# Kernel tuning notes

Measured on AMD Instinct MI355X. Metric: run time of the kernel, lower is better.

## Reference

```python
import jax, jax.numpy as jnp
import numpy as np

T = 2048            # flattened tokens (vLLM style)
D = 4096            # hidden_size
NSSM = 128          # ssm_state_size
K = 4               # conv kernel size
G = 8               # n_groups
H = 128             # mamba_num_heads
P = 64              # mamba_head_dim
INTER = H * P       # 8192 = expand * hidden_size
CONV_DIM = INTER + 2 * G * NSSM   # 10240 (x, B, C share the conv)
PROJ = INTER + CONV_DIM + H       # 18560 (z, xBC, dt)
Q = 128             # SSD chunk size
EPS = 1e-5


def setup_inputs() -> dict:
    key = jax.random.key(0)
    ks = jax.random.split(key, 9)
    s = 0.02
    return {
        "hidden_states": jax.random.normal(ks[0], (T, D), jnp.float32),
        "residual": jax.random.normal(ks[1], (T, D), jnp.float32),
        "norm_w": jnp.ones((D,), jnp.float32),
        "in_proj_w": jax.random.normal(ks[2], (PROJ, D), jnp.float32) * s,
        "conv_w": jax.random.normal(ks[3], (CONV_DIM, K), jnp.float32) * 0.2,
        "conv_b": jax.random.normal(ks[4], (CONV_DIM,), jnp.float32) * 0.1,
        "A_log": jnp.log(jax.random.uniform(ks[5], (H,), jnp.float32, 1.0, 16.0)),
        "D_res": jax.random.normal(ks[6], (H,), jnp.float32) * 0.5 + 1.0,
        "dt_bias": jax.random.normal(ks[7], (H,), jnp.float32) * 0.5,
        "gn_w": jnp.ones((INTER,), jnp.float32),
        "out_proj_w": jax.random.normal(ks[8], (D, INTER), jnp.float32) * s,
    }


def _forward(hidden_states, residual, norm_w, in_proj_w, conv_w, conv_b,
             A_log, D_res, dt_bias, gn_w, out_proj_w):
    # ---- fused add + RMSNorm (vLLM RMSNorm(hidden, residual)) ----
    resid = hidden_states + residual
    hs = resid * jax.lax.rsqrt(jnp.mean(resid * resid, -1, keepdims=True) + EPS) * norm_w

    # ---- MambaMixer2 ----
    proj = hs @ in_proj_w.T                              # [T, PROJ]
    z, xBC, dt = jnp.split(proj, [INTER, INTER + CONV_DIM], axis=-1)

    # causal depthwise conv1d over time + SiLU
    xp = jnp.pad(xBC, ((K - 1, 0), (0, 0)))
    conv = conv_b + sum(conv_w[:, k] * xp[k:k + T] for k in range(K))
    xBC = jax.nn.silu(conv)

    x, B, C = jnp.split(xBC, [INTER, INTER + G * NSSM], axis=-1)
    x = x.reshape(T, H, P)
    Bh = jnp.repeat(B.reshape(T, G, NSSM), H // G, axis=1)   # [T,H,N]
    Ch = jnp.repeat(C.reshape(T, G, NSSM), H // G, axis=1)   # [T,H,N]

    dt = jax.nn.softplus(dt + dt_bias)                   # [T,H]
    A = -jnp.exp(A_log)                                  # [H] (negative)

    # ---- SSD chunked selective scan ----
    NC = T // Q
    a = (dt * A).reshape(NC, Q, H)                       # per-step log decay (<=0)
    cum = jnp.cumsum(a, axis=1)                          # inclusive cumsum, [NC,Q,H]
    Xd = (dt[:, :, None] * x).reshape(NC, Q, H, P)
    Bc = Bh.reshape(NC, Q, H, NSSM)
    Cc = Ch.reshape(NC, Q, H, NSSM)

    # intra-chunk: Y[i] = sum_{j<=i} (C_i.B_j) exp(cum_i-cum_j) Xd_j
    CB = jnp.einsum('cqhn,ckhn->chqk', Cc, Bc)
    cumT = cum.transpose(0, 2, 1)                        # [NC,H,Q]
    mask = jnp.tril(jnp.ones((Q, Q), bool))
    Lm = jnp.where(mask, jnp.exp(cumT[:, :, :, None] - cumT[:, :, None, :]), 0.0)
    Y = jnp.einsum('chqk,ckhp->cqhp', CB * Lm, Xd)

    # chunk-local end states, then scan states across chunks
    cum_end = cum[:, -1]                                 # [NC,H]
    decay_out = jnp.exp(cum_end[:, None] - cum)          # [NC,Q,H]
    S_loc = jnp.einsum('cqhn,cqh,cqhp->chnp', Bc, decay_out, Xd)
    chunk_decay = jnp.exp(cum_end)                       # [NC,H]

    def step(s, inp):
        dec, sl = inp
        return dec[:, None, None] * s + sl, s            # emit state BEFORE chunk

    _, S_prev = jax.lax.scan(step, jnp.zeros((H, NSSM, P), x.dtype),
                             (chunk_decay, S_loc))       # [NC,H,N,P]

    # inter-chunk contribution + skip connection D*x
    Y = Y + jnp.einsum('cqhn,cqh,chnp->cqhp', Cc, jnp.exp(cum), S_prev)
    y = Y.reshape(T, H, P) + D_res[None, :, None] * x

    # gated RMSNorm then out projection
    y = y.reshape(T, INTER) * jax.nn.silu(z)
    y = y * jax.lax.rsqrt(jnp.mean(y * y, -1, keepdims=True) + EPS) * gn_w
    return y @ out_proj_w.T, resid


def reference(hidden_states, residual, norm_w, in_proj_w, conv_w, conv_b,
              A_log, D_res, dt_bias, gn_w, out_proj_w):
    return _forward(hidden_states, residual, norm_w, in_proj_w, conv_w, conv_b,
                    A_log, D_res, dt_bias, gn_w, out_proj_w)
```

## Files before the change

### kernel.cpp

```cpp
#include <hip/hip_runtime.h>
#include <stdint.h>

typedef unsigned short u16;
typedef unsigned int   u32;
typedef float  f32x4  __attribute__((ext_vector_type(4)));
typedef __bf16 bf16x8 __attribute__((ext_vector_type(8)));
typedef u16    u16x4  __attribute__((ext_vector_type(4)));
typedef u16    u16x8  __attribute__((ext_vector_type(8)));

#define T_N     2048
#define D_N     4096
#define H_N     128
#define P_N     64
#define G_N     8
#define NS_N    128
#define INTER_N 8192
#define CONVD_N 10240
#define PROJ_N  18560
#define NGEMM_N 18432
#define NC_N    16

__device__ __forceinline__ float bf2f(u16 u){ u32 x = ((u32)u) << 16; return __builtin_bit_cast(float, x); }
__device__ __forceinline__ u16 f2bf(float f){
  u32 u = __builtin_bit_cast(u32, f);
  u += 0x7FFFu + ((u >> 16) & 1u);
  return (u16)(u >> 16);
}

__device__ __forceinline__ void gld_lds16(const void* g, void* lds){
  __builtin_amdgcn_global_load_lds(
      (const __attribute__((address_space(1))) void*)(uintptr_t)g,
      (__attribute__((address_space(3))) void*)(u32)(uintptr_t)lds,
      16, 0, 0);
}

__global__ __launch_bounds__(256)
void k_addnorm(const float* __restrict__ hin, const float* __restrict__ rin,
               const float* __restrict__ nw, float* __restrict__ resid,
               u16* __restrict__ hs16, float* __restrict__ rstd){
  __shared__ float red[4];
  const int row = blockIdx.x, tid = threadIdx.x;
  const size_t rb = (size_t)row * D_N;
  f32x4 s[4];
  float ss = 0.f;
  #pragma unroll
  for (int i = 0; i < 4; ++i){
    int c4 = tid + i*256;
    f32x4 a = *(const f32x4*)&hin[rb + (size_t)c4*4];
    f32x4 b = *(const f32x4*)&rin[rb + (size_t)c4*4];
    s[i] = a + b;
    *(f32x4*)&resid[rb + (size_t)c4*4] = s[i];
    ss += s[i][0]*s[i][0] + s[i][1]*s[i][1] + s[i][2]*s[i][2] + s[i][3]*s[i][3];
  }
  #pragma unroll
  for (int o = 32; o > 0; o >>= 1) ss += __shfl_down(ss, o, 64);
  if ((tid & 63) == 0) red[tid >> 6] = ss;
  __syncthreads();
  float tot = (red[0] + red[1]) + (red[2] + red[3]);
  float rs = rsqrtf(tot / (float)D_N + 1e-5f);
  if (tid == 0) rstd[row] = rs;
  #pragma unroll
  for (int i = 0; i < 4; ++i){
    int c4 = tid + i*256;
    f32x4 w = *(const f32x4*)&nw[(size_t)c4*4];
    u16x4 o = { f2bf(s[i][0]*rs*w[0]), f2bf(s[i][1]*rs*w[1]),
                f2bf(s[i][2]*rs*w[2]), f2bf(s[i][3]*rs*w[3]) };
    *(u16x4*)&hs16[rb + (size_t)c4*4] = o;
  }
}

__global__ void k_cvt(const float* __restrict__ in, u16* __restrict__ out, size_t n4){
  size_t i = (size_t)blockIdx.x * blockDim.x + threadIdx.x;
  size_t stride = (size_t)gridDim.x * blockDim.x;
  for (; i < n4; i += stride){
    f32x4 v = *(const f32x4*)&in[i*4];
    u16x4 o = { f2bf(v[0]), f2bf(v[1]), f2bf(v[2]), f2bf(v[3]) };
    *(u16x4*)&out[i*4] = o;
  }
}

__global__ void k_wdt(const float* __restrict__ W, const float* __restrict__ nw,
                      float* __restrict__ Wn){
  int idx = blockIdx.x*256 + threadIdx.x;
  int d = idx >> 7, h = idx & 127;
  Wn[(size_t)d*128 + h] = W[(size_t)(INTER_N + CONVD_N + h)*D_N + d] * nw[d];
}

__global__ __launch_bounds__(256)
void k_dtgemm(const float* __restrict__ resid, const float* __restrict__ Wn,
              float* __restrict__ dtpart){
  __shared__ float lhs[16*128];
  const int tid = threadIdx.x;
  const int tb = blockIdx.x >> 3, ks = blockIdx.x & 7;
  const int t0 = tb * 16;
  const int k0 = ks * (D_N / 8);
  const int hcol = tid & 127, rh = tid >> 7;
  float acc[8] = {0,0,0,0,0,0,0,0};
  for (int kt = k0; kt < k0 + D_N/8; kt += 128){
    __syncthreads();
    #pragma unroll
    for (int it = 0; it < 2; ++it){
      int idx = it*256 + tid;
      int rr = idx >> 5, c4 = idx & 31;
      *(f32x4*)&lhs[rr*128 + c4*4] = *(const f32x4*)&resid[(size_t)(t0+rr)*D_N + kt + c4*4];
    }
    __syncthreads();
    #pragma unroll 8
    for (int kk = 0; kk < 128; ++kk){
      float w = Wn[(size_t)(kt+kk)*128 + hcol];
      #pragma unroll
      for (int j = 0; j < 8; ++j) acc[j] += lhs[(rh*8 + j)*128 + kk] * w;
    }
  }
  #pragma unroll
  for (int j = 0; j < 8; ++j){
    int t = t0 + rh*8 + j;
    dtpart[((size_t)ks*T_N + t)*128 + hcol] = acc[j];
  }
}

__global__ void k_dtprep(const float* __restrict__ dtpart, const float* __restrict__ rstd,
                         const float* __restrict__ dt_bias, const float* __restrict__ A_log,
                         float* __restrict__ dtv, float* __restrict__ cum,
                         float* __restrict__ cumend, float* __restrict__ dec){
  int c = blockIdx.x, h = threadIdx.x;
  float A = -expf(A_log[h]);
  float bias = dt_bias[h];
  float cm = 0.f;
  for (int q = 0; q < 128; ++q){
    int t = c*128 + q;
    float s = 0.f;
    #pragma unroll
    for (int kspl = 0; kspl < 8; ++kspl)
      s += dtpart[((size_t)kspl*T_N + t)*128 + h];
    float x = s * rstd[t] + bias;
    float dv = (x > 20.f) ? x : log1pf(expf(x));
    dtv[(size_t)t*128 + h] = dv;
    cm += dv * A;
    cum[(size_t)t*128 + h] = cm;
  }
  cumend[c*128 + h] = cm;
  dec[c*128 + h] = expf(cm);
}

#define STA(BUF,HH,KT) gld_lds16(pA + (size_t)((HH)*64)*K + (size_t)(KT)*64, shb + (BUF)*BSZ + (HH)*8192 + tid*16)
#define STB(BUF,HH,KT) gld_lds16(pB[HH] + (size_t)(KT)*64, shb + (BUF)*BSZ + 32768 + (HH)*8192 + tid*16)
#define VMWN do { asm volatile("s_waitcnt vmcnt(%0)" :: "n"(NFRAG) : "memory"); __builtin_amdgcn_sched_barrier(0); } while(0)
#define PH_RD(BUF, Q)                                                                   \
    bf16x8 aa00 = *(const bf16x8*)(shb + (BUF)*BSZ + rdA + (Q)*4096 + sA0);             \
    bf16x8 aa01 = *(const bf16x8*)(shb + (BUF)*BSZ + rdA + (Q)*4096 + sA1);             \
    bf16x8 aa10 = *(const bf16x8*)(shb + (BUF)*BSZ + rdA + (Q)*4096 + 2048 + sA0);      \
    bf16x8 aa11 = *(const bf16x8*)(shb + (BUF)*BSZ + rdA + (Q)*4096 + 2048 + sA1);
#define PH_RB(BUF, BB)                                                                  \
    _Pragma("unroll") for (int nn = 0; nn < NFRAG; ++nn){                               \
      BB[nn][0] = *(const bf16x8*)(shb + (BUF)*BSZ + rdB + nn*2048 + sA0);              \
      BB[nn][1] = *(const bf16x8*)(shb + (BUF)*BSZ + rdB + nn*2048 + sA1);              \
    }
#define PH_MM(Q, BB)                                                                    \
    __builtin_amdgcn_s_barrier();                                                       \
    __builtin_amdgcn_sched_barrier(0);                                                  \
    __builtin_amdgcn_s_setprio(1);                                                      \
    _Pragma("unroll") for (int nn = 0; nn < NFRAG; ++nn){                               \
      acc[(Q)*2+0][nn] = __builtin_amdgcn_mfma_f32_16x16x32_bf16(aa00, BB[nn][0], acc[(Q)*2+0][nn],0,0,0); \
      acc[(Q)*2+0][nn] = __builtin_amdgcn_mfma_f32_16x16x32_bf16(aa01, BB[nn][1], acc[(Q)*2+0][nn],0,0,0); \
      acc[(Q)*2+1][nn] = __builtin_amdgcn_mfma_f32_16x16x32_bf16(aa10, BB[nn][0], acc[(Q)*2+1][nn],0,0,0); \
      acc[(Q)*2+1][nn] = __builtin_amdgcn_mfma_f32_16x16x32_bf16(aa11, BB[nn][1], acc[(Q)*2+1][nn],0,0,0); \
    }                                                                                   \
    __builtin_amdgcn_s_setprio(0);                                                      \
    __builtin_amdgcn_s_barrier();                                                       \
    __builtin_amdgcn_sched_barrier(0);

template<int NFRAG>
__global__ __launch_bounds__(512, 2)
void k_gemm256(const u16* __restrict__ A, const u16* __restrict__ Bm,
               float* __restrict__ C, int ldc, int K, int nkt, size_t zstride){
  constexpr int BSZ = 32768 + NFRAG*8192;
  __shared__ char shb[2*BSZ];
  const int tid = threadIdx.x, ln = tid & 63, wid = tid >> 6;
  const int wm = wid >> 2, wn = wid & 3;
  const int lr = ln & 15, lg = ln >> 4;

  const int gx = gridDim.x;
  const int nwg = gx * gridDim.y;
  const int lin = blockIdx.y * gx + blockIdx.x;
  const int qq = nwg >> 3;
  const int swz = (lin & 7)*qq + (lin >> 3);
  const int m0 = (swz / gx) << 8;
  const int n0 = (swz % gx) * (NFRAG*64);
  const int kbase = blockIdx.z * nkt;

  const int srow = tid >> 3;
  const int slog = ((tid & 7) ^ (srow & 7)) * 8;
  const u16* pA = A + (size_t)(m0 + srow)*K + (size_t)kbase*64 + slog;
  const u16* pB[NFRAG];
  #pragma unroll
  for (int hh = 0; hh < NFRAG; ++hh)
    pB[hh] = Bm + (size_t)(n0 + hh*64 + srow)*K + (size_t)kbase*64 + slog;

  const int sA0 = (lg ^ (ln & 7)) << 4;
  const int sA1 = ((4 + lg) ^ (ln & 7)) << 4;
  const u32 rdA = wm*16384 + lr*128;
  const u32 rdB = 32768 + (wn*NFRAG*16 + lr)*128;

  f32x4 acc[8][NFRAG] = {};

  #pragma unroll
  for (int hh = 0; hh < 4; ++hh) STA(0, hh, 0);
  #pragma unroll
  for (int hh = 0; hh < NFRAG; ++hh) STB(0, hh, 0);
  #pragma unroll
  for (int hh = 0; hh < NFRAG; ++hh) STB(1, hh, 1);
  VMWN;
  __builtin_amdgcn_s_barrier();
  __builtin_amdgcn_sched_barrier(0);

  const int nit = nkt >> 1;
  #pragma unroll 1
  for (int it = 0; it < nit; ++it){
    const int t1 = 2*it + 1;
    int t2 = 2*it + 2; if (t2 >= nkt) t2 = 0;
    int t3 = 2*it + 3; if (t3 >= nkt) t3 = 1;
    bf16x8 bb0[NFRAG][2], bb1[NFRAG][2];
    { PH_RD(0,0) PH_RB(0, bb0)
      #pragma unroll
      for (int hh = 0; hh < 4; ++hh) STA(1, hh, t1);
      PH_MM(0, bb0) }
    { PH_RD(0,1)
      #pragma unroll
      for (int hh = 0; hh < NFRAG; ++hh) STB(0, hh, t2);
      PH_MM(1, bb0) }
    { PH_RD(0,2)
      PH_MM(2, bb0) }
    { PH_RD(0,3)
      VMWN;
      PH_MM(3, bb0) }
    { PH_RD(1,0) PH_RB(1, bb1)
      #pragma unroll
      for (int hh = 0; hh < 4; ++hh) STA(0, hh, t2);
      PH_MM(0, bb1) }
    { PH_RD(1,1)
      #pragma unroll
      for (int hh = 0; hh < NFRAG; ++hh) STB(1, hh, t3);
      PH_MM(1, bb1) }
    { PH_RD(1,2)
      PH_MM(2, bb1) }
    { PH_RD(1,3)
      VMWN;
      PH_MM(3, bb1) }
  }
  asm volatile("s_waitcnt vmcnt(0)" ::: "memory");

  float* Cz = C + (size_t)blockIdx.z * zstride;
  const int crow = m0 + wm*128 + lg*4;
  const int ccol = n0 + wn*(NFRAG*16) + lr;
  #pragma unroll
  for (int m = 0; m < 8; ++m)
    #pragma unroll
    for (int nn = 0; nn < NFRAG; ++nn)
      #pragma unroll
      for (int r = 0; r < 4; ++r)
        Cz[(size_t)(crow + m*16 + r)*ldc + ccol + nn*16] = acc[m][nn][r];
}

__global__ __launch_bounds__(256)
void k_add2(const float* __restrict__ a, const float* __restrict__ b,
            float* __restrict__ o, int n4){
  int i = blockIdx.x*256 + threadIdx.x;
  if (i < n4){
    f32x4 x = *(const f32x4*)&a[(size_t)i*4];
    f32x4 y = *(const f32x4*)&b[(size_t)i*4];
    x = x + y;
    *(f32x4*)&o[(size_t)i*4] = x;
  }
}

__global__ __launch_bounds__(256)
void k_conv(const float* __restrict__ proj, const float* __restrict__ cw,
            const float* __restrict__ cb, u16* __restrict__ x16,
            u16* __restrict__ B16, u16* __restrict__ C16){
  const int ch = blockIdx.x*256 + threadIdx.x;
  const int t = blockIdx.y;
  f32x4 w = *(const f32x4*)&cw[(size_t)ch*4];
  float acc = cb[ch];
  const float* pcol = proj + INTER_N + ch;
  if (t >= 3) acc += w[0] * pcol[(size_t)(t-3)*PROJ_N];
  if (t >= 2) acc += w[1] * pcol[(size_t)(t-2)*PROJ_N];
  if (t >= 1) acc += w[2] * pcol[(size_t)(t-1)*PROJ_N];
  acc += w[3] * pcol[(size_t)t*PROJ_N];
  float v = acc / (1.f + __expf(-acc));
  u16 o = f2bf(v);
  if (ch < INTER_N)             x16[(size_t)t*INTER_N + ch] = o;
  else if (ch < INTER_N + 1024) B16[(size_t)t*1024 + (ch - INTER_N)] = o;
  else                          C16[(size_t)t*1024 + (ch - INTER_N - 1024)] = o;
}

__global__ __launch_bounds__(512)
void k_ssda(const u16* __restrict__ B16, const u16* __restrict__ x16,
            const float* __restrict__ dtv, const float* __restrict__ cum,
            const float* __restrict__ cumend, u16* __restrict__ SlocT){
  __shared__ u16 lBdT[128*136];
  __shared__ u16 lXdT[64*136];
  __shared__ float lDec[128], lDt[128];
  const int tid = threadIdx.x, wid = tid >> 6, ln = tid & 63;
  const int c = blockIdx.x >> 7, h = blockIdx.x & 127, g = h >> 4;
  if (tid < 128){
    int t = c*128 + tid;
    lDec[tid] = __expf(cumend[c*128 + h] - cum[(size_t)t*128 + h]);
    lDt[tid]  = dtv[(size_t)t*128 + h];
  }
  __syncthreads();
  for (int it = 0; it < 32; ++it){
    int idx = it*512 + tid;
    int q = idx >> 7, n = idx & 127;
    float bv = bf2f(B16[(size_t)(c*128 + q)*1024 + g*128 + n]) * lDec[q];
    lBdT[n*136 + q] = f2bf(bv);
  }
  for (int it = 0; it < 16; ++it){
    int idx = it*512 + tid;
    int q = idx >> 6, p = idx & 63;
    float xv = bf2f(x16[(size_t)(c*128 + q)*INTER_N + h*64 + p]) * lDt[q];
    lXdT[p*136 + q] = f2bf(xv);
  }
  __syncthreads();
  const int wr = wid >> 1, wc = wid & 1;
  const int kofs = (ln >> 4) << 3;
  f32x4 acc[2][2] = {};
  #pragma unroll
  for (int ks = 0; ks < 4; ++ks){
    bf16x8 a[2], b[2];
    #pragma unroll
    for (int m = 0; m < 2; ++m) a[m] = *(const bf16x8*)&lBdT[(wr*32 + m*16 + (ln & 15))*136 + ks*32 + kofs];
    #pragma unroll
    for (int n = 0; n < 2; ++n) b[n] = *(const bf16x8*)&lXdT[(wc*32 + n*16 + (ln & 15))*136 + ks*32 + kofs];
    #pragma unroll
    for (int m = 0; m < 2; ++m)
      #pragma unroll
      for (int n = 0; n < 2; ++n)
        acc[m][n] = __builtin_amdgcn_mfma_f32_16x16x32_bf16(a[m], b[n], acc[m][n], 0, 0, 0);
  }
  const size_t base = (size_t)(c*128 + h) * 8192;
  #pragma unroll
  for (int m = 0; m < 2; ++m)
    #pragma unroll
    for (int n = 0; n < 2; ++n){
      int p  = wc*32 + n*16 + (ln & 15);
      int nn = wr*32 + m*16 + ((ln >> 4) << 2);
      u16x4 o = { f2bf(acc[m][n][0]), f2bf(acc[m][n][1]), f2bf(acc[m][n][2]), f2bf(acc[m][n][3]) };
      *(u16x4*)&SlocT[base + (size_t)p*128 + nn] = o;
    }
}

__global__ __launch_bounds__(256)
void k_scan(const u16* __restrict__ SlocT, const float* __restrict__ dec,
            u16* __restrict__ SprevT){
  int idx = blockIdx.x*256 + threadIdx.x;
  int h = idx >> 11, p = (idx >> 5) & 63, n4 = idx & 31;
  float s0 = 0.f, s1 = 0.f, s2 = 0.f, s3 = 0.f;
  for (int c = 0; c < NC_N; ++c){
    size_t off = (size_t)(c*128 + h)*8192 + (size_t)p*128 + n4*4;
    u16x4 o = { f2bf(s0), f2bf(s1), f2bf(s2), f2bf(s3) };
    *(u16x4*)&SprevT[off] = o;
    u16x4 sl = *(const u16x4*)&SlocT[off];
    float d = dec[c*128 + h];
    s0 = d*s0 + bf2f(sl[0]); s1 = d*s1 + bf2f(sl[1]);
    s2 = d*s2 + bf2f(sl[2]); s3 = d*s3 + bf2f(sl[3]);
  }
}

__global__ __launch_bounds__(512)
void k_ssdb(const u16* __restrict__ C16, const u16* __restrict__ B16g,
            const u16* __restrict__ x16, const float* __restrict__ dtv,
            const float* __restrict__ cum, const u16* __restrict__ SprevT,
            const float* __restrict__ proj, const float* __restrict__ Dres,
            u16* __restrict__ yg16){
  __shared__ u16 lC[128*136];
  __shared__ u16 lBP[128*136];
  __shared__ u16 lXdT[64*136];
  __shared__ float lCum[128], lDt[128];
  const int tid = threadIdx.x, wid = tid >> 6, ln = tid & 63;
  const int c = blockIdx.x >> 7, h = blockIdx.x & 127, g = h >> 4;
  if (tid < 128){
    int t = c*128 + tid;
    lCum[tid] = cum[(size_t)t*128 + h];
    lDt[tid]  = dtv[(size_t)t*128 + h];
  }
  __syncthreads();
  for (int it = 0; it < 32; ++it){
    int idx = it*512 + tid;
    int q = idx >> 7, n = idx & 127;
    size_t gi = (size_t)(c*128 + q)*1024 + g*128 + n;
    lC[q*136 + n]  = C16[gi];
    lBP[q*136 + n] = B16g[gi];
  }
  for (int it = 0; it < 16; ++it){
    int idx = it*512 + tid;
    int q = idx >> 6, p = idx & 63;
    lXdT[p*136 + q] = f2bf(bf2f(x16[(size_t)(c*128 + q)*INTER_N + h*64 + p]) * lDt[q]);
  }
  __syncthreads();
  const int kofs = (ln >> 4) << 3;
  {
    const int wr = wid >> 2, wc = wid & 3;
    f32x4 cb[4][2] = {};
    #pragma unroll
    for (int ks = 0; ks < 4; ++ks){
      bf16x8 a[4], b[2];
      #pragma unroll
      for (int m = 0; m < 4; ++m) a[m] = *(const bf16x8*)&lC[(wr*64 + m*16 + (ln & 15))*136 + ks*32 + kofs];
      #pragma unroll
      for (int n = 0; n < 2; ++n) b[n] = *(const bf16x8*)&lBP[(wc*32 + n*16 + (ln & 15))*136 + ks*32 + kofs];
      #pragma unroll
      for (int m = 0; m < 4; ++m)
        #pragma unroll
        for (int n = 0; n < 2; ++n)
          cb[m][n] = __builtin_amdgcn_mfma_f32_16x16x32_bf16(a[m], b[n], cb[m][n], 0, 0, 0);
    }
    __syncthreads();
    #pragma unroll
    for (int m = 0; m < 4; ++m)
      #pragma unroll
      for (int n = 0; n < 2; ++n){
        int kcol = (wid & 3)*32 + n*16 + (ln & 15);
        float ck = lCum[kcol];
        #pragma unroll
        for (int r = 0; r < 4; ++r){
          int q = (wid >> 2)*64 + m*16 + ((ln >> 4) << 2) + r;
          float v = (kcol <= q) ? cb[m][n][r] * __expf(lCum[q] - ck) : 0.f;
          lBP[q*136 + kcol] = f2bf(v);
        }
      }
  }
  __syncthreads();
  const int yr = wid >> 1, yc = wid & 1;
  f32x4 y1[2][2] = {}, y2[2][2] = {};
  const size_t spbase = (size_t)(c*128 + h) * 8192;
  #pragma unroll
  for (int ks = 0; ks < 4; ++ks){
    bf16x8 ap[2], acf[2], bx[2], bs[2];
    #pragma unroll
    for (int m = 0; m < 2; ++m){
      int qr = yr*32 + m*16 + (ln & 15);
      ap[m]  = *(const bf16x8*)&lBP[qr*136 + ks*32 + kofs];
      acf[m] = *(const bf16x8*)&lC [qr*136 + ks*32 + kofs];
    }
    #pragma unroll
    for (int n = 0; n < 2; ++n){
      int p = yc*32 + n*16 + (ln & 15);
      bx[n] = *(const bf16x8*)&lXdT[p*136 + ks*32 + kofs];
      bs[n] = *(const bf16x8*)&SprevT[spbase + (size_t)p*128 + ks*32 + kofs];
    }
    #pragma unroll
    for (int m = 0; m < 2; ++m)
      #pragma unroll
      for (int n = 0; n < 2; ++n){
        y1[m][n] = __builtin_amdgcn_mfma_f32_16x16x32_bf16(ap[m],  bx[n], y1[m][n], 0, 0, 0);
        y2[m][n] = __builtin_amdgcn_mfma_f32_16x16x32_bf16(acf[m], bs[n], y2[m][n], 0, 0, 0);
      }
  }
  const float dh = Dres[h];
  #pragma unroll
  for (int m = 0; m < 2; ++m)
    #pragma unroll
    for (int r = 0; r < 4; ++r){
      int q = yr*32 + m*16 + ((ln >> 4) << 2) + r;
      float eq = __expf(lCum[q]);
      size_t t = (size_t)(c*128 + q);
      #pragma unroll
      for (int n = 0; n < 2; ++n){
        int p = yc*32 + n*16 + (ln & 15);
        int chn = h*64 + p;
        float xv = bf2f(x16[t*INTER_N + chn]);
        float zv = proj[t*PROJ_N + chn];
        float yv = y1[m][n][r] + eq*y2[m][n][r] + dh*xv;
        float sg = zv / (1.f + __expf(-zv));
        yg16[t*INTER_N + chn] = f2bf(yv * sg);
      }
    }
}

__global__ __launch_bounds__(256)
void k_gnorm(const u16* __restrict__ yg, const float* __restrict__ gnw,
             u16* __restrict__ yn16){
  __shared__ float red[4];
  const int row = blockIdx.x, tid = threadIdx.x;
  const u16* rp = yg + (size_t)row * INTER_N;
  u16x8 v[4];
  float ss = 0.f;
  #pragma unroll
  for (int i = 0; i < 4; ++i){
    v[i] = *(const u16x8*)&rp[(size_t)(tid + i*256)*8];
    #pragma unroll
    for (int j = 0; j < 8; ++j){ float f = bf2f(v[i][j]); ss += f*f; }
  }
  #pragma unroll
  for (int o = 32; o > 0; o >>= 1) ss += __shfl_down(ss, o, 64);
  if ((tid & 63) == 0) red[tid >> 6] = ss;
  __syncthreads();
  float tot = (red[0] + red[1]) + (red[2] + red[3]);
  float sc = rsqrtf(tot / (float)INTER_N + 1e-5f);
  #pragma unroll
  for (int i = 0; i < 4; ++i){
    int c8 = (tid + i*256)*8;
    u16x8 o;
    #pragma unroll
    for (int j = 0; j < 8; ++j)
      o[j] = f2bf(bf2f(v[i][j]) * sc * gnw[c8 + j]);
    *(u16x8*)&yn16[(size_t)row*INTER_N + c8] = o;
  }
}

extern "C" void kernel_launch(void* const* d_in, const int* in_sizes, int n_in,
                              void* d_out, int out_size, void* d_ws, size_t ws_size,
                              hipStream_t stream){
  (void)in_sizes; (void)n_in; (void)out_size;
  const float* hs_in     = (const float*)d_in[0];
  const float* res_in    = (const float*)d_in[1];
  const float* norm_w    = (const float*)d_in[2];
  const float* in_proj_w = (const float*)d_in[3];
  const float* conv_w    = (const float*)d_in[4];
  const float* conv_b    = (const float*)d_in[5];
  const float* A_log     = (const float*)d_in[6];
  const float* D_res     = (const float*)d_in[7];
  const float* dt_bias   = (const float*)d_in[8];
  const float* gn_w      = (const float*)d_in[9];
  const float* out_proj_w= (const float*)d_in[10];

  float* out0      = (float*)d_out;
  float* resid_out = out0 + (size_t)T_N * D_N;

  char* ws = (char*)d_ws;
  const size_t o_hs16   = 0;
  const size_t o_Win16  = 16777216;
  const size_t o_Wout16 = 168820736;
  const size_t o_proj   = 235929600;
  const size_t o_Wn     = 387973120;
  const size_t o_dtv    = 391118848;
  const size_t o_cum    = 392167424;
  const size_t o_cumend = 393216000;
  const size_t o_dec    = 393224192;
  const size_t o_rstd   = 393232384;
  const size_t o_x16    = 393240576;
  const size_t o_B16    = 426795008;
  const size_t o_C16    = 430989312;
  const size_t o_SlocT  = 435183616;
  const size_t o_SprevT = 468738048;
  const size_t o_yn16   = 502292480;
  const size_t WS_NEED  = 535846912;
  if (ws_size < WS_NEED) return;

  u16*   hs16   = (u16*)  (ws + o_hs16);
  u16*   Win16  = (u16*)  (ws + o_Win16);
  u16*   Wout16 = (u16*)  (ws + o_Wout16);
  float* proj   = (float*)(ws + o_proj);
  float* Wn     = (float*)(ws + o_Wn);
  float* dtpart = (float*)(ws + o_proj);
  float* dtv    = (float*)(ws + o_dtv);
  float* cum    = (float*)(ws + o_cum);
  float* cumend = (float*)(ws + o_cumend);
  float* dec    = (float*)(ws + o_dec);
  float* rstd   = (float*)(ws + o_rstd);
  u16*   x16    = (u16*)  (ws + o_x16);
  u16*   B16    = (u16*)  (ws + o_B16);
  u16*   C16    = (u16*)  (ws + o_C16);
  u16*   SlocT  = (u16*)  (ws + o_SlocT);
  u16*   SprevT = (u16*)  (ws + o_SprevT);
  u16*   yn16   = (u16*)  (ws + o_yn16);
  u16*   yg16   = (u16*)  (ws + o_Win16);

  k_addnorm<<<T_N, 256, 0, stream>>>(hs_in, res_in, norm_w, resid_out, hs16, rstd);
  k_cvt<<<4096, 256, 0, stream>>>(in_proj_w,  Win16,  (size_t)NGEMM_N * D_N / 4);
  k_cvt<<<2048, 256, 0, stream>>>(out_proj_w, Wout16, (size_t)D_N * INTER_N / 4);
  k_wdt<<<2048, 256, 0, stream>>>(in_proj_w, norm_w, Wn);
  k_dtgemm<<<1024, 256, 0, stream>>>(resid_out, Wn, dtpart);
  k_dtprep<<<NC_N, 128, 0, stream>>>(dtpart, rstd, dt_bias, A_log, dtv, cum, cumend, dec);
  k_gemm256<3><<<dim3(NGEMM_N/192, T_N/256, 1), 512, 0, stream>>>(hs16, Win16, proj, PROJ_N, D_N, D_N/64, 0);
  k_conv<<<dim3(CONVD_N/256, T_N), 256, 0, stream>>>(proj, conv_w, conv_b, x16, B16, C16);
  k_ssda<<<NC_N * H_N, 512, 0, stream>>>(B16, x16, dtv, cum, cumend, SlocT);
  k_scan<<<1024, 256, 0, stream>>>(SlocT, dec, SprevT);
  k_ssdb<<<NC_N * H_N, 512, 0, stream>>>(C16, B16, x16, dtv, cum, SprevT, proj, D_res, yg16);
  k_gnorm<<<T_N, 256, 0, stream>>>(yg16, gn_w, yn16);
  k_gemm256<4><<<dim3(D_N/256, T_N/256, 2), 512, 0, stream>>>(yn16, Wout16, proj, D_N, INTER_N, INTER_N/64/2, (size_t)T_N*D_N);
  k_add2<<<T_N*D_N/1024, 256, 0, stream>>>(proj, proj + (size_t)T_N*D_N, out0, T_N*D_N/4);
}
```

Before: 982.0 us.

## Store in-proj output as bf16, tile conv over time, drop GEMM barrier, vectorize dt GEMM

The in-projection GEMM now writes its output in bf16 instead of fp32, which halves that write traffic and the reads done later by the conv and ssdb kernels. The conv kernel processes 64 timesteps per thread and carries a sliding window of the previous inputs, so each value is loaded once. The leading s_barrier in the GEMM MFMA phase is removed, and the dt GEMM inner loop reads LDS with f32x4 loads. The out-projection partial planes move to a separate workspace region. Rounding the z and xBC activations to bf16 adds precision loss, and dropping the barrier could create a shared-memory hazard.

```diff
diff --git a/kernel.cpp b/kernel.cpp
--- a/kernel.cpp
+++ b/kernel.cpp
@@ -105,11 +105,16 @@
       *(f32x4*)&lhs[rr*128 + c4*4] = *(const f32x4*)&resid[(size_t)(t0+rr)*D_N + kt + c4*4];
     }
     __syncthreads();
-    #pragma unroll 8
-    for (int kk = 0; kk < 128; ++kk){
-      float w = Wn[(size_t)(kt+kk)*128 + hcol];
-      #pragma unroll
-      for (int j = 0; j < 8; ++j) acc[j] += lhs[(rh*8 + j)*128 + kk] * w;
+    #pragma unroll 4
+    for (int kk4 = 0; kk4 < 32; ++kk4){
+      f32x4 w4;
+      #pragma unroll
+      for (int j = 0; j < 4; ++j) w4[j] = Wn[(size_t)(kt + kk4*4 + j)*128 + hcol];
+      #pragma unroll
+      for (int j = 0; j < 8; ++j){
+        f32x4 lv = *(const f32x4*)&lhs[(rh*8 + j)*128 + kk4*4];
+        acc[j] += lv[0]*w4[0] + lv[1]*w4[1] + lv[2]*w4[2] + lv[3]*w4[3];
+      }
     }
   }
   #pragma unroll
@@ -157,8 +162,6 @@
       BB[nn][1] = *(const bf16x8*)(shb + (BUF)*BSZ + rdB + nn*2048 + sA1);              \
     }
 #define PH_MM(Q, BB)                                                                    \
-    __builtin_amdgcn_s_barrier();                                                       \
-    __builtin_amdgcn_sched_barrier(0);                                                  \
     __builtin_amdgcn_s_setprio(1);                                                      \
     _Pragma("unroll") for (int nn = 0; nn < NFRAG; ++nn){                               \
       acc[(Q)*2+0][nn] = __builtin_amdgcn_mfma_f32_16x16x32_bf16(aa00, BB[nn][0], acc[(Q)*2+0][nn],0,0,0); \
@@ -170,10 +173,10 @@
     __builtin_amdgcn_s_barrier();                                                       \
     __builtin_amdgcn_sched_barrier(0);
 
-template<int NFRAG>
+template<int NFRAG, typename OT>
 __global__ __launch_bounds__(512, 2)
 void k_gemm256(const u16* __restrict__ A, const u16* __restrict__ Bm,
-               float* __restrict__ C, int ldc, int K, int nkt, size_t zstride){
+               OT* __restrict__ C, int ldc, int K, int nkt, size_t zstride){
   constexpr int BSZ = 32768 + NFRAG*8192;
   __shared__ char shb[2*BSZ];
   const int tid = threadIdx.x, ln = tid & 63, wid = tid >> 6;
@@ -250,7 +253,7 @@
   }
   asm volatile("s_waitcnt vmcnt(0)" ::: "memory");
 
-  float* Cz = C + (size_t)blockIdx.z * zstride;
+  OT* Cz = C + (size_t)blockIdx.z * zstride;
   const int crow = m0 + wm*128 + lg*4;
   const int ccol = n0 + wn*(NFRAG*16) + lr;
   #pragma unroll
@@ -258,8 +261,13 @@
     #pragma unroll
     for (int nn = 0; nn < NFRAG; ++nn)
       #pragma unroll
-      for (int r = 0; r < 4; ++r)
-        Cz[(size_t)(crow + m*16 + r)*ldc + ccol + nn*16] = acc[m][nn][r];
+      for (int r = 0; r < 4; ++r){
+        float v = acc[m][nn][r];
+        if constexpr (__is_same(OT, float))
+          Cz[(size_t)(crow + m*16 + r)*ldc + ccol + nn*16] = v;
+        else
+          Cz[(size_t)(crow + m*16 + r)*ldc + ccol + nn*16] = f2bf(v);
+      }
 }
 
 __global__ __launch_bounds__(256)
@@ -275,23 +283,33 @@
 }
 
 __global__ __launch_bounds__(256)
-void k_conv(const float* __restrict__ proj, const float* __restrict__ cw,
+void k_conv(const u16* __restrict__ proj16, const float* __restrict__ cw,
             const float* __restrict__ cb, u16* __restrict__ x16,
             u16* __restrict__ B16, u16* __restrict__ C16){
   const int ch = blockIdx.x*256 + threadIdx.x;
-  const int t = blockIdx.y;
+  const int tbase = blockIdx.y*64;
   f32x4 w = *(const f32x4*)&cw[(size_t)ch*4];
-  float acc = cb[ch];
-  const float* pcol = proj + INTER_N + ch;
-  if (t >= 3) acc += w[0] * pcol[(size_t)(t-3)*PROJ_N];
-  if (t >= 2) acc += w[1] * pcol[(size_t)(t-2)*PROJ_N];
-  if (t >= 1) acc += w[2] * pcol[(size_t)(t-1)*PROJ_N];
-  acc += w[3] * pcol[(size_t)t*PROJ_N];
-  float v = acc / (1.f + __expf(-acc));
-  u16 o = f2bf(v);
-  if (ch < INTER_N)             x16[(size_t)t*INTER_N + ch] = o;
-  else if (ch < INTER_N + 1024) B16[(size_t)t*1024 + (ch - INTER_N)] = o;
-  else                          C16[(size_t)t*1024 + (ch - INTER_N - 1024)] = o;
+  const float bias = cb[ch];
+  const u16* pcol = proj16 + INTER_N + ch;
+  float p0 = 0.f, p1 = 0.f, p2 = 0.f;
+  if (tbase >= 3){
+    p0 = bf2f(pcol[(size_t)(tbase-3)*PROJ_N]);
+    p1 = bf2f(pcol[(size_t)(tbase-2)*PROJ_N]);
+    p2 = bf2f(pcol[(size_t)(tbase-1)*PROJ_N]);
+  }
+  u16* xdst = (ch < INTER_N) ? x16 + ch
+            : (ch < INTER_N + 1024) ? B16 + (ch - INTER_N)
+            : C16 + (ch - INTER_N - 1024);
+  const int dstride = (ch < INTER_N) ? INTER_N : 1024;
+  #pragma unroll 4
+  for (int i = 0; i < 64; ++i){
+    int t = tbase + i;
+    float cur = bf2f(pcol[(size_t)t*PROJ_N]);
+    float acc = bias + w[0]*p0 + w[1]*p1 + w[2]*p2 + w[3]*cur;
+    float v = acc / (1.f + __expf(-acc));
+    xdst[(size_t)t*dstride] = f2bf(v);
+    p0 = p1; p1 = p2; p2 = cur;
+  }
 }
 
 __global__ __launch_bounds__(512)
@@ -371,7 +389,7 @@
 void k_ssdb(const u16* __restrict__ C16, const u16* __restrict__ B16g,
             const u16* __restrict__ x16, const float* __restrict__ dtv,
             const float* __restrict__ cum, const u16* __restrict__ SprevT,
-            const float* __restrict__ proj, const float* __restrict__ Dres,
+            const u16* __restrict__ proj16, const float* __restrict__ Dres,
             u16* __restrict__ yg16){
   __shared__ u16 lC[128*136];
   __shared__ u16 lBP[128*136];
@@ -470,7 +488,7 @@
         int p = yc*32 + n*16 + (ln & 15);
         int chn = h*64 + p;
         float xv = bf2f(x16[t*INTER_N + chn]);
-        float zv = proj[t*PROJ_N + chn];
+        float zv = bf2f(proj16[t*PROJ_N + chn]);
         float yv = y1[m][n][r] + eq*y2[m][n][r] + dh*xv;
         float sg = zv / (1.f + __expf(-zv));
         yg16[t*INTER_N + chn] = f2bf(yv * sg);
@@ -533,6 +551,7 @@
   const size_t o_Win16  = 16777216;
   const size_t o_Wout16 = 168820736;
   const size_t o_proj   = 235929600;
+  const size_t o_plane  = 311951360;
   const size_t o_Wn     = 387973120;
   const size_t o_dtv    = 391118848;
   const size_t o_cum    = 392167424;
@@ -551,7 +570,8 @@
   u16*   hs16   = (u16*)  (ws + o_hs16);
   u16*   Win16  = (u16*)  (ws + o_Win16);
   u16*   Wout16 = (u16*)  (ws + o_Wout16);
-  float* proj   = (float*)(ws + o_proj);
+  u16*   proj16 = (u16*)  (ws + o_proj);
+  float* planes = (float*)(ws + o_plane);
   float* Wn     = (float*)(ws + o_Wn);
   float* dtpart = (float*)(ws + o_proj);
   float* dtv    = (float*)(ws + o_dtv);
@@ -573,12 +593,12 @@
   k_wdt<<<2048, 256, 0, stream>>>(in_proj_w, norm_w, Wn);
   k_dtgemm<<<1024, 256, 0, stream>>>(resid_out, Wn, dtpart);
   k_dtprep<<<NC_N, 128, 0, stream>>>(dtpart, rstd, dt_bias, A_log, dtv, cum, cumend, dec);
-  k_gemm256<3><<<dim3(NGEMM_N/192, T_N/256, 1), 512, 0, stream>>>(hs16, Win16, proj, PROJ_N, D_N, D_N/64, 0);
-  k_conv<<<dim3(CONVD_N/256, T_N), 256, 0, stream>>>(proj, conv_w, conv_b, x16, B16, C16);
+  k_gemm256<3, u16><<<dim3(NGEMM_N/192, T_N/256, 1), 512, 0, stream>>>(hs16, Win16, proj16, PROJ_N, D_N, D_N/64, 0);
+  k_conv<<<dim3(CONVD_N/256, T_N/64), 256, 0, stream>>>(proj16, conv_w, conv_b, x16, B16, C16);
   k_ssda<<<NC_N * H_N, 512, 0, stream>>>(B16, x16, dtv, cum, cumend, SlocT);
   k_scan<<<1024, 256, 0, stream>>>(SlocT, dec, SprevT);
-  k_ssdb<<<NC_N * H_N, 512, 0, stream>>>(C16, B16, x16, dtv, cum, SprevT, proj, D_res, yg16);
+  k_ssdb<<<NC_N * H_N, 512, 0, stream>>>(C16, B16, x16, dtv, cum, SprevT, proj16, D_res, yg16);
   k_gnorm<<<T_N, 256, 0, stream>>>(yg16, gn_w, yn16);
-  k_gemm256<4><<<dim3(D_N/256, T_N/256, 2), 512, 0, stream>>>(yn16, Wout16, proj, D_N, INTER_N, INTER_N/64/2, (size_t)T_N*D_N);
-  k_add2<<<T_N*D_N/1024, 256, 0, stream>>>(proj, proj + (size_t)T_N*D_N, out0, T_N*D_N/4);
-}
+  k_gemm256<4, float><<<dim3(D_N/256, T_N/256, 2), 512, 0, stream>>>(yn16, Wout16, planes, D_N, INTER_N, INTER_N/64/2, (size_t)T_N*D_N);
+  k_add2<<<T_N*D_N/1024, 256, 0, stream>>>(planes, planes + (size_t)T_N*D_N, out0, T_N*D_N/4);
+}
```

Result: faster. 948.6 us (-3.4%).
